# Kernel optimization log

Hardware: AMD Instinct MI355X
Metric: run time of the kernel (lower is better)

The kernel has to match this reference:

```python
import jax, jax.numpy as jnp
import numpy as np

N, E, D_IN, H, C = 40000, 640000, 128, 2, 64  # nodes, edges, in_channels, heads, out_channels


def setup_inputs() -> dict:
    key = jax.random.key(0)
    ks = jax.random.split(key, 8)
    x = jax.random.normal(ks[0], (N, D_IN), jnp.float32)
    edge_attr = jax.random.normal(ks[1], (E, D_IN), jnp.float32)
    edge_index = jax.random.randint(ks[2], (2, E), 0, N, dtype=jnp.int32)
    W_msg = jax.random.normal(ks[3], (D_IN, H * C), jnp.float32) / np.sqrt(D_IN)
    b_msg = jnp.zeros((H * C,), jnp.float32)
    W_edge = jax.random.normal(ks[4], (D_IN, H * C), jnp.float32) / np.sqrt(D_IN)
    b_edge = jnp.zeros((H * C,), jnp.float32)
    W_self = jax.random.normal(ks[5], (D_IN, C), jnp.float32) / np.sqrt(D_IN)
    b_self = jnp.zeros((C,), jnp.float32)
    att_msg = jax.random.normal(ks[6], (1, H, C), jnp.float32) / np.sqrt(C)
    return dict(x=x, edge_attr=edge_attr, W_msg=W_msg, b_msg=b_msg,
                W_edge=W_edge, b_edge=b_edge, W_self=W_self, b_self=b_self,
                att_msg=att_msg, edge_index=edge_index)


def reference(x, edge_attr, W_msg, b_msg, W_edge, b_edge, W_self, b_self, att_msg, edge_index):
    src, dst = edge_index[0], edge_index[1]
    # edge feature transform (also returned as updated edge_attr)
    le = edge_attr @ W_edge + b_edge                      # [E, H*C]
    # gather source nodes -> linear message + edge term (message_basic)
    m = x[src] @ W_msg + b_msg + le                       # [E, H*C]
    m = m.reshape(E, H, C)
    # additive attention: alpha = leaky_relu((m * att_msg).sum(-1))
    alpha = jax.nn.leaky_relu(jnp.sum(m * att_msg, axis=-1), 0.2)  # [E, H]
    # PyG scatter-softmax over destination segments
    amax = jax.ops.segment_max(alpha, dst, num_segments=N)        # [N, H]
    amax = jnp.where(jnp.isfinite(amax), amax, 0.0)
    ex = jnp.exp(alpha - amax[dst])
    denom = jax.ops.segment_sum(ex, dst, num_segments=N)
    a = ex / (denom[dst] + 1e-16)                                  # [E, H]
    # weighted scatter-add aggregation (aggr='add')
    agg = jax.ops.segment_sum(m * a[..., None], dst, num_segments=N)  # [N, H, C]
    # mean over heads + self linear (in_channels != out_channels -> Linear)
    out = agg.mean(axis=1) + (x @ W_self + b_self)                 # [N, C]
    return out, le
```

## Files before the change

kernel.cpp:

```cpp
#include <hip/hip_runtime.h>

#define N_NODES 40000
#define N_EDGES 640000

typedef __attribute__((ext_vector_type(8))) short short8;
typedef __attribute__((ext_vector_type(4))) float float4v;

__device__ inline short f2bf(float f) {
  unsigned u = __float_as_uint(f);
  unsigned r = (u + 0x7FFFu + ((u >> 16) & 1u)) >> 16;
  return (short)r;
}

__global__ void prep_w(const float* __restrict__ Wm, const float* __restrict__ We,
                       const float* __restrict__ Ws, short* __restrict__ WtM,
                       short* __restrict__ WtE, short* __restrict__ WtS) {
  int i = blockIdx.x * 256 + threadIdx.x;
  if (i < 16384) {
    int c = i >> 7, k = i & 127;
    WtM[c * 128 + k] = f2bf(Wm[k * 128 + c]);
  } else if (i < 32768) {
    int j = i - 16384;
    int c = j >> 7, k = j & 127;
    WtE[c * 128 + k] = f2bf(We[k * 128 + c]);
  } else {
    int j = i - 32768;
    int c = j >> 7, k = j & 127;
    WtS[c * 128 + k] = f2bf(Ws[k * 64 + c]);
  }
}

template <int NT>
__global__ __launch_bounds__(256) void gemm_rows(const float* __restrict__ A,
                                                 const short* __restrict__ Wt,
                                                 const float* __restrict__ bias,
                                                 float* __restrict__ out) {
  __shared__ short wt[NT * 16 * 136];
  for (int i = threadIdx.x; i < NT * 16 * 16; i += 256) {
    int c = i >> 4, j = i & 15;
    *(uint4*)&wt[c * 136 + j * 8] = ((const uint4*)Wt)[i];
  }
  __syncthreads();
  const int l = threadIdx.x & 63, w = threadIdx.x >> 6;
  const int lr = l & 15, q = l >> 4;
  const int row = blockIdx.x * 64 + w * 16 + lr;
  float4v acc[NT];
#pragma unroll
  for (int t = 0; t < NT; ++t) acc[t] = (float4v){0.f, 0.f, 0.f, 0.f};
  const float* ap = A + (size_t)row * 128 + q * 8;
#pragma unroll
  for (int s = 0; s < 4; ++s) {
    float4 a0 = *(const float4*)(ap + s * 32);
    float4 a1 = *(const float4*)(ap + s * 32 + 4);
    short8 af;
    af[0] = f2bf(a0.x); af[1] = f2bf(a0.y); af[2] = f2bf(a0.z); af[3] = f2bf(a0.w);
    af[4] = f2bf(a1.x); af[5] = f2bf(a1.y); af[6] = f2bf(a1.z); af[7] = f2bf(a1.w);
#pragma unroll
    for (int t = 0; t < NT; ++t) {
      short8 bf = *(const short8*)&wt[(t * 16 + lr) * 136 + s * 32 + q * 8];
      acc[t] = __builtin_amdgcn_mfma_f32_16x16x32_bf16(af, bf, acc[t], 0, 0, 0);
    }
  }
  const int orow = blockIdx.x * 64 + w * 16 + q * 4;
#pragma unroll
  for (int t = 0; t < NT; ++t) {
    int col = lr + 16 * t;
    float b = bias[col];
#pragma unroll
    for (int j = 0; j < 4; ++j)
      out[(size_t)(orow + j) * (NT * 16) + col] = acc[t][j] + b;
  }
}

__global__ __launch_bounds__(256) void edge_kernel(
    const float* __restrict__ ea, const short* __restrict__ WtE,
    const float* __restrict__ b_edge, const float* __restrict__ xm,
    const float* __restrict__ att, const int* __restrict__ src,
    float* __restrict__ le_out, float* __restrict__ alpha_out) {
  __shared__ short wt[128 * 136];
  __shared__ int sid[64];
  for (int i = threadIdx.x; i < 128 * 16; i += 256) {
    int c = i >> 4, j = i & 15;
    *(uint4*)&wt[c * 136 + j * 8] = ((const uint4*)WtE)[i];
  }
  if (threadIdx.x < 64) sid[threadIdx.x] = src[blockIdx.x * 64 + threadIdx.x];
  __syncthreads();
  const int l = threadIdx.x & 63, w = threadIdx.x >> 6;
  const int lr = l & 15, q = l >> 4;
  const int r0 = blockIdx.x * 64 + w * 16;
  float4v acc[8];
#pragma unroll
  for (int t = 0; t < 8; ++t) acc[t] = (float4v){0.f, 0.f, 0.f, 0.f};
  const float* ap = ea + (size_t)(r0 + lr) * 128 + q * 8;
#pragma unroll
  for (int s = 0; s < 4; ++s) {
    float4 a0 = *(const float4*)(ap + s * 32);
    float4 a1 = *(const float4*)(ap + s * 32 + 4);
    short8 af;
    af[0] = f2bf(a0.x); af[1] = f2bf(a0.y); af[2] = f2bf(a0.z); af[3] = f2bf(a0.w);
    af[4] = f2bf(a1.x); af[5] = f2bf(a1.y); af[6] = f2bf(a1.z); af[7] = f2bf(a1.w);
#pragma unroll
    for (int t = 0; t < 8; ++t) {
      short8 bf = *(const short8*)&wt[(t * 16 + lr) * 136 + s * 32 + q * 8];
      acc[t] = __builtin_amdgcn_mfma_f32_16x16x32_bf16(af, bf, acc[t], 0, 0, 0);
    }
  }
  const int rb = q * 4;
  int sidr[4];
#pragma unroll
  for (int j = 0; j < 4; ++j) sidr[j] = sid[w * 16 + rb + j];
  float p[8];
#pragma unroll
  for (int k = 0; k < 8; ++k) p[k] = 0.f;
#pragma unroll
  for (int t = 0; t < 8; ++t) {
    int col = lr + 16 * t;
    float b = b_edge[col];
    float av = att[col];
    int hp = (t >> 2) * 4;
#pragma unroll
    for (int j = 0; j < 4; ++j) {
      float lev = acc[t][j] + b;
      le_out[(size_t)(r0 + rb + j) * 128 + col] = lev;
      float mv = lev + xm[(size_t)sidr[j] * 128 + col];
      p[hp + j] += mv * av;
    }
  }
#pragma unroll
  for (int d = 1; d < 16; d <<= 1) {
#pragma unroll
    for (int k = 0; k < 8; ++k) p[k] += __shfl_xor(p[k], d);
  }
  if (lr < 8) {
    int j = lr >> 1, h = lr & 1;
    float v = p[h * 4 + j];
    alpha_out[(size_t)(r0 + rb + j) * 2 + h] = v > 0.f ? v : 0.2f * v;
  }
}

__device__ inline unsigned enc_f(float v) {
  unsigned u = __float_as_uint(v);
  return (u & 0x80000000u) ? ~u : (u | 0x80000000u);
}
__device__ inline float dec_f(unsigned u) {
  unsigned v = (u & 0x80000000u) ? (u & 0x7FFFFFFFu) : ~u;
  return __uint_as_float(v);
}

__global__ void amax_k(const float* __restrict__ alpha, const int* __restrict__ dst,
                       unsigned* __restrict__ amx) {
  int i = blockIdx.x * 256 + threadIdx.x;
  int e = i >> 1, h = i & 1;
  atomicMax(&amx[dst[e] * 2 + h], enc_f(alpha[i]));
}

__global__ void denom_k(float* __restrict__ alpha, const int* __restrict__ dst,
                        const unsigned* __restrict__ amx, float* __restrict__ den) {
  int i = blockIdx.x * 256 + threadIdx.x;
  int e = i >> 1, h = i & 1;
  int d = dst[e];
  float mx = dec_f(amx[d * 2 + h]);
  float ex = __expf(alpha[i] - mx);
  alpha[i] = ex;
  unsafeAtomicAdd(&den[d * 2 + h], ex);
}

__global__ __launch_bounds__(256) void agg_k(const float* __restrict__ le,
                                             const float* __restrict__ xm,
                                             const float* __restrict__ ex,
                                             const float* __restrict__ den,
                                             const int* __restrict__ src,
                                             const int* __restrict__ dst,
                                             float* __restrict__ agg) {
  int w = threadIdx.x >> 6, l = threadIdx.x & 63;
  int e = blockIdx.x * 4 + w;
  int s = src[e], d = dst[e];
  float a0 = ex[e * 2 + 0] / (den[d * 2 + 0] + 1e-16f);
  float a1 = ex[e * 2 + 1] / (den[d * 2 + 1] + 1e-16f);
  float m0 = le[(size_t)e * 128 + l] + xm[(size_t)s * 128 + l];
  float m1 = le[(size_t)e * 128 + 64 + l] + xm[(size_t)s * 128 + 64 + l];
  unsafeAtomicAdd(&agg[(size_t)d * 64 + l], 0.5f * (m0 * a0 + m1 * a1));
}

__global__ void out_k(const float* __restrict__ agg, const float* __restrict__ xs,
                      float* __restrict__ out) {
  int i = blockIdx.x * 256 + threadIdx.x;
  float4 a = ((const float4*)agg)[i];
  float4 s = ((const float4*)xs)[i];
  float4 r;
  r.x = a.x + s.x; r.y = a.y + s.y; r.z = a.z + s.z; r.w = a.w + s.w;
  ((float4*)out)[i] = r;
}

extern "C" void kernel_launch(void* const* d_in, const int* in_sizes, int n_in,
                              void* d_out, int out_size, void* d_ws, size_t ws_size,
                              hipStream_t stream) {
  const float* x      = (const float*)d_in[0];
  const float* ea     = (const float*)d_in[1];
  const float* W_msg  = (const float*)d_in[2];
  const float* b_msg  = (const float*)d_in[3];
  const float* W_edge = (const float*)d_in[4];
  const float* b_edge = (const float*)d_in[5];
  const float* W_self = (const float*)d_in[6];
  const float* b_self = (const float*)d_in[7];
  const float* att    = (const float*)d_in[8];
  const int*   eidx   = (const int*)d_in[9];
  const int* src = eidx;
  const int* dst = eidx + N_EDGES;
  float* out_p = (float*)d_out;
  float* le_p  = out_p + (size_t)N_NODES * 64;

  char* ws = (char*)d_ws;
  short* WtM   = (short*)(ws);
  short* WtE   = (short*)(ws + 32768);
  short* WtS   = (short*)(ws + 65536);
  float* xm    = (float*)(ws + 81920);
  float* xs    = (float*)(ws + 20561920);
  float* alp   = (float*)(ws + 30801920);
  unsigned* amx = (unsigned*)(ws + 35921920);
  float* den   = (float*)(ws + 36241920);
  float* agg   = (float*)(ws + 36561920);

  hipMemsetAsync(ws + 35921920, 0, 10880000, stream);

  prep_w<<<160, 256, 0, stream>>>(W_msg, W_edge, W_self, WtM, WtE, WtS);
  gemm_rows<8><<<625, 256, 0, stream>>>(x, WtM, b_msg, xm);
  gemm_rows<4><<<625, 256, 0, stream>>>(x, WtS, b_self, xs);
  edge_kernel<<<10000, 256, 0, stream>>>(ea, WtE, b_edge, xm, att, src, le_p, alp);
  amax_k<<<5000, 256, 0, stream>>>(alp, dst, amx);
  denom_k<<<5000, 256, 0, stream>>>(alp, dst, amx, den);
  agg_k<<<160000, 256, 0, stream>>>(le_p, xm, alp, den, src, dst, agg);
  out_k<<<2500, 256, 0, stream>>>(agg, xs, out_p);
}
```

Measured before the change: 828.6 us.

## Replace atomic scatter softmax/aggregation with CSR-sorted per-node gather aggregation

Builds a destination-sorted CSR (histogram with atomic ranks, single-block scan, scatter of edge ids). A per-node wavefront kernel then computes the segment max, the softmax denominator and the weighted sum by gathering its incoming edges, and fuses the self-linear add into the output write. This removes the float atomics on max, denominator and aggregation and the separate output kernel. In exchange it adds three small preprocessing kernels, a serial single-block scan, and irregular gathers with load imbalance across node degrees.

```diff
diff --git a/kernel.cpp b/kernel.cpp
--- a/kernel.cpp
+++ b/kernel.cpp
@@ -138,58 +138,98 @@
   }
 }
 
-__device__ inline unsigned enc_f(float v) {
-  unsigned u = __float_as_uint(v);
-  return (u & 0x80000000u) ? ~u : (u | 0x80000000u);
-}
-__device__ inline float dec_f(unsigned u) {
-  unsigned v = (u & 0x80000000u) ? (u & 0x7FFFFFFFu) : ~u;
-  return __uint_as_float(v);
-}
-
-__global__ void amax_k(const float* __restrict__ alpha, const int* __restrict__ dst,
-                       unsigned* __restrict__ amx) {
-  int i = blockIdx.x * 256 + threadIdx.x;
-  int e = i >> 1, h = i & 1;
-  atomicMax(&amx[dst[e] * 2 + h], enc_f(alpha[i]));
-}
-
-__global__ void denom_k(float* __restrict__ alpha, const int* __restrict__ dst,
-                        const unsigned* __restrict__ amx, float* __restrict__ den) {
-  int i = blockIdx.x * 256 + threadIdx.x;
-  int e = i >> 1, h = i & 1;
-  int d = dst[e];
-  float mx = dec_f(amx[d * 2 + h]);
-  float ex = __expf(alpha[i] - mx);
-  alpha[i] = ex;
-  unsafeAtomicAdd(&den[d * 2 + h], ex);
-}
-
-__global__ __launch_bounds__(256) void agg_k(const float* __restrict__ le,
-                                             const float* __restrict__ xm,
-                                             const float* __restrict__ ex,
-                                             const float* __restrict__ den,
-                                             const int* __restrict__ src,
-                                             const int* __restrict__ dst,
-                                             float* __restrict__ agg) {
-  int w = threadIdx.x >> 6, l = threadIdx.x & 63;
-  int e = blockIdx.x * 4 + w;
-  int s = src[e], d = dst[e];
-  float a0 = ex[e * 2 + 0] / (den[d * 2 + 0] + 1e-16f);
-  float a1 = ex[e * 2 + 1] / (den[d * 2 + 1] + 1e-16f);
-  float m0 = le[(size_t)e * 128 + l] + xm[(size_t)s * 128 + l];
-  float m1 = le[(size_t)e * 128 + 64 + l] + xm[(size_t)s * 128 + 64 + l];
-  unsafeAtomicAdd(&agg[(size_t)d * 64 + l], 0.5f * (m0 * a0 + m1 * a1));
-}
-
-__global__ void out_k(const float* __restrict__ agg, const float* __restrict__ xs,
-                      float* __restrict__ out) {
-  int i = blockIdx.x * 256 + threadIdx.x;
-  float4 a = ((const float4*)agg)[i];
-  float4 s = ((const float4*)xs)[i];
-  float4 r;
-  r.x = a.x + s.x; r.y = a.y + s.y; r.z = a.z + s.z; r.w = a.w + s.w;
-  ((float4*)out)[i] = r;
+
+__global__ void hist_k(const int* __restrict__ dst, int* __restrict__ cnt,
+                       int* __restrict__ rank) {
+  int e = blockIdx.x * 256 + threadIdx.x;
+  rank[e] = atomicAdd(&cnt[dst[e]], 1);
+}
+
+__global__ __launch_bounds__(1024) void scan_k(const int* __restrict__ cnt,
+                                               int* __restrict__ ofs) {
+  __shared__ int tsum[1024];
+  const int t = threadIdx.x;
+  const int b = t * 40;
+  const int hi = min(b + 40, N_NODES);
+  int s = 0;
+  for (int i = b; i < hi; ++i) s += cnt[i];
+  tsum[t] = s;
+  __syncthreads();
+  for (int d = 1; d < 1024; d <<= 1) {
+    int v = (t >= d) ? tsum[t - d] : 0;
+    __syncthreads();
+    tsum[t] += v;
+    __syncthreads();
+  }
+  int run = (t == 0) ? 0 : tsum[t - 1];
+  for (int i = b; i < hi; ++i) { ofs[i] = run; run += cnt[i]; }
+  if (t == 1023) ofs[N_NODES] = run;
+}
+
+__global__ void scatter_k(const int* __restrict__ dst, const int* __restrict__ ofs,
+                          const int* __restrict__ rank, int* __restrict__ eid) {
+  int e = blockIdx.x * 256 + threadIdx.x;
+  eid[ofs[dst[e]] + rank[e]] = e;
+}
+
+__global__ __launch_bounds__(256) void node_agg(
+    const float* __restrict__ le, const float* __restrict__ xm,
+    const float* __restrict__ alp, const float* __restrict__ xs,
+    const int* __restrict__ ofs, const int* __restrict__ eid,
+    const int* __restrict__ src, float* __restrict__ out) {
+  const int w = threadIdx.x >> 6, l = threadIdx.x & 63;
+  const int n = blockIdx.x * 4 + w;
+  const int beg = ofs[n];
+  const int deg = ofs[n + 1] - beg;
+  float acc = 0.f;
+  if (deg > 0) {
+    float m0 = -1e30f, m1 = -1e30f;
+    for (int i = l; i < deg; i += 64) {
+      int e = eid[beg + i];
+      m0 = fmaxf(m0, alp[2 * e]);
+      m1 = fmaxf(m1, alp[2 * e + 1]);
+    }
+#pragma unroll
+    for (int d = 1; d < 64; d <<= 1) {
+      m0 = fmaxf(m0, __shfl_xor(m0, d));
+      m1 = fmaxf(m1, __shfl_xor(m1, d));
+    }
+    float s0 = 0.f, s1 = 0.f;
+    for (int i = l; i < deg; i += 64) {
+      int e = eid[beg + i];
+      s0 += __expf(alp[2 * e] - m0);
+      s1 += __expf(alp[2 * e + 1] - m1);
+    }
+#pragma unroll
+    for (int d = 1; d < 64; d <<= 1) {
+      s0 += __shfl_xor(s0, d);
+      s1 += __shfl_xor(s1, d);
+    }
+    const float r0 = 1.f / (s0 + 1e-16f);
+    const float r1 = 1.f / (s1 + 1e-16f);
+    for (int base = 0; base < deg; base += 64) {
+      int i = base + l;
+      int eR = 0, sR = 0;
+      float w0R = 0.f, w1R = 0.f;
+      if (i < deg) {
+        eR = eid[beg + i];
+        sR = src[eR];
+        w0R = __expf(alp[2 * eR] - m0) * r0;
+        w1R = __expf(alp[2 * eR + 1] - m1) * r1;
+      }
+      const int c = min(64, deg - base);
+      for (int j = 0; j < c; ++j) {
+        int e = __shfl(eR, j);
+        int s = __shfl(sR, j);
+        float w0 = __shfl(w0R, j);
+        float w1 = __shfl(w1R, j);
+        float v0 = le[(size_t)e * 128 + l] + xm[(size_t)s * 128 + l];
+        float v1 = le[(size_t)e * 128 + 64 + l] + xm[(size_t)s * 128 + 64 + l];
+        acc += w0 * v0 + w1 * v1;
+      }
+    }
+  }
+  out[(size_t)n * 64 + l] = 0.5f * acc + xs[(size_t)n * 64 + l];
 }
 
 extern "C" void kernel_launch(void* const* d_in, const int* in_sizes, int n_in,
@@ -211,24 +251,25 @@
   float* le_p  = out_p + (size_t)N_NODES * 64;
 
   char* ws = (char*)d_ws;
-  short* WtM   = (short*)(ws);
-  short* WtE   = (short*)(ws + 32768);
-  short* WtS   = (short*)(ws + 65536);
-  float* xm    = (float*)(ws + 81920);
-  float* xs    = (float*)(ws + 20561920);
-  float* alp   = (float*)(ws + 30801920);
-  unsigned* amx = (unsigned*)(ws + 35921920);
-  float* den   = (float*)(ws + 36241920);
-  float* agg   = (float*)(ws + 36561920);
-
-  hipMemsetAsync(ws + 35921920, 0, 10880000, stream);
+  short* WtM  = (short*)(ws);
+  short* WtE  = (short*)(ws + 32768);
+  short* WtS  = (short*)(ws + 65536);
+  float* xm   = (float*)(ws + 81920);
+  float* xs   = (float*)(ws + 20561920);
+  float* alp  = (float*)(ws + 30801920);
+  int*   cnt  = (int*)(ws + 35921920);
+  int*   ofs  = (int*)(ws + 36081920);
+  int*   rank = (int*)(ws + 36241936);
+  int*   eid  = (int*)(ws + 38801936);
+
+  hipMemsetAsync(cnt, 0, 160000, stream);
 
   prep_w<<<160, 256, 0, stream>>>(W_msg, W_edge, W_self, WtM, WtE, WtS);
   gemm_rows<8><<<625, 256, 0, stream>>>(x, WtM, b_msg, xm);
   gemm_rows<4><<<625, 256, 0, stream>>>(x, WtS, b_self, xs);
+  hist_k<<<2500, 256, 0, stream>>>(dst, cnt, rank);
+  scan_k<<<1, 1024, 0, stream>>>(cnt, ofs);
+  scatter_k<<<2500, 256, 0, stream>>>(dst, ofs, rank, eid);
   edge_kernel<<<10000, 256, 0, stream>>>(ea, WtE, b_edge, xm, att, src, le_p, alp);
-  amax_k<<<5000, 256, 0, stream>>>(alp, dst, amx);
-  denom_k<<<5000, 256, 0, stream>>>(alp, dst, amx, den);
-  agg_k<<<160000, 256, 0, stream>>>(le_p, xm, alp, den, src, dst, agg);
-  out_k<<<2500, 256, 0, stream>>>(agg, xs, out_p);
-}
+  node_agg<<<10000, 256, 0, stream>>>(le_p, xm, alp, xs, ofs, eid, src, out_p);
+}
```

Result: no change. 814.0 us (-1.8%).
